# Kernel tuning notes

Hardware: AMD Instinct MI355X
Metric: run time of the kernel (lower is better)

## Reference

```python
import jax, jax.numpy as jnp
from jax import lax
import numpy as np

IMG = 1024
STRIDES = (4, 8, 16, 32, 64)
FEAT_HW = (256, 128, 64, 32, 16)
ANCHOR_SCALE = 8.0          # per-level scale multiplier of stride
RATIOS = (0.5, 1.0, 2.0)
N_ANCHOR = len(RATIOS)
PRE_NMS = 6000
POST_NMS = 300
NMS_THRESH = 0.7
MIN_SIZE = 16.0
IMG_SCALE = 1.0
NEG = -1e9


def _conv(x, w, b, pad):
    y = lax.conv_general_dilated(x, w, (1, 1), [(pad, pad), (pad, pad)],
                                 dimension_numbers=("NCHW", "OIHW", "NCHW"))
    return y + b[None, :, None, None]


def _level_anchors(H, W, stride):
    # base anchors (ymin,xmin,ymax,xmax) centered at 0, one scale per level
    r = jnp.asarray(RATIOS, jnp.float32)
    hs = stride * ANCHOR_SCALE * jnp.sqrt(r)
    ws = stride * ANCHOR_SCALE * jnp.sqrt(1.0 / r)
    base = jnp.stack([-hs / 2, -ws / 2, hs / 2, ws / 2], axis=1)  # [A,4]
    ys = jnp.arange(H, dtype=jnp.float32) * stride
    xs = jnp.arange(W, dtype=jnp.float32) * stride
    gy, gx = jnp.meshgrid(ys, xs, indexing="ij")
    shift = jnp.stack([gy, gx, gy, gx], axis=-1).reshape(-1, 1, 4)   # [HW,1,4]
    return (shift + base[None, :, :]).reshape(-1, 4)                 # [HW*A,4]


def _decode(anchors, loc):
    ah = anchors[:, 2] - anchors[:, 0]
    aw = anchors[:, 3] - anchors[:, 1]
    acy = anchors[:, 0] + 0.5 * ah
    acx = anchors[:, 1] + 0.5 * aw
    dy, dx, dh, dw = loc[:, 0], loc[:, 1], loc[:, 2], loc[:, 3]
    cy = dy * ah + acy
    cx = dx * aw + acx
    h = jnp.exp(dh) * ah
    w = jnp.exp(dw) * aw
    boxes = jnp.stack([cy - 0.5 * h, cx - 0.5 * w, cy + 0.5 * h, cx + 0.5 * w], axis=1)
    return jnp.clip(boxes, 0.0, float(IMG))


def _iou_row(box, boxes):
    ty = jnp.maximum(box[0], boxes[:, 0])
    tx = jnp.maximum(box[1], boxes[:, 1])
    by = jnp.minimum(box[2], boxes[:, 2])
    bx = jnp.minimum(box[3], boxes[:, 3])
    inter = jnp.maximum(by - ty, 0.0) * jnp.maximum(bx - tx, 0.0)
    a1 = (box[2] - box[0]) * (box[3] - box[1])
    a2 = (boxes[:, 2] - boxes[:, 0]) * (boxes[:, 3] - boxes[:, 1])
    return inter / jnp.maximum(a1 + a2 - inter, 1e-9)


def _nms(boxes, scores):
    n = boxes.shape[0]
    idx_range = jnp.arange(n)

    def body(sc, _):
        i = jnp.argmax(sc)
        valid = sc[i] > NEG / 2
        iou = _iou_row(boxes[i], boxes)
        new_sc = jnp.where((iou > NMS_THRESH) | (idx_range == i), NEG, sc)
        sc = jnp.where(valid, new_sc, sc)
        return sc, (i, valid)

    _, (idx, keep) = lax.scan(body, scores, None, length=POST_NMS)
    return boxes[idx] * keep[:, None].astype(boxes.dtype)


def reference(p2, p3, p4, p5, p6, conv_w, conv_b, loc_w, loc_b, score_w, score_b):
    feats = [p2, p3, p4, p5, p6]
    locs, fgs, anchors = [], [], []
    for f, stride in zip(feats, STRIDES):
        h = jax.nn.relu(_conv(f, conv_w, conv_b, 1))
        loc = _conv(h, loc_w, loc_b, 0)        # [1,4A,H,W]
        sc = _conv(h, score_w, score_b, 0)     # [1,2A,H,W]
        H, W = loc.shape[2], loc.shape[3]
        loc = loc.transpose(0, 2, 3, 1).reshape(-1, 4)          # [HWA,4]
        sc = sc.transpose(0, 2, 3, 1).reshape(-1, 2)            # [HWA,2]
        fgs.append(jax.nn.softmax(sc, axis=-1)[:, 1])
        locs.append(loc)
        anchors.append(_level_anchors(H, W, stride))
    loc = jnp.concatenate(locs, axis=0)
    fg = jnp.concatenate(fgs, axis=0)
    anc = jnp.concatenate(anchors, axis=0)

    boxes = _decode(anc, loc)
    hh = boxes[:, 2] - boxes[:, 0]
    ww = boxes[:, 3] - boxes[:, 1]
    min_sz = MIN_SIZE * IMG_SCALE
    fg = jnp.where((hh >= min_sz) & (ww >= min_sz), fg, NEG)

    top_scores, top_idx = lax.top_k(fg, PRE_NMS)
    top_boxes = boxes[top_idx]
    rois = _nms(top_boxes, top_scores)   # [POST_NMS,4]
    return rois


def setup_inputs() -> dict:
    key = jax.random.key(0)
    ks = jax.random.split(key, 11)
    inp = {}
    for i, (name, hw) in enumerate(zip(["p2", "p3", "p4", "p5", "p6"], FEAT_HW)):
        inp[name] = jax.random.normal(ks[i], (1, 256, hw, hw), jnp.float32)
    inp["conv_w"] = 0.01 * jax.random.normal(ks[5], (256, 256, 3, 3), jnp.float32)
    inp["conv_b"] = jnp.zeros((256,), jnp.float32)
    inp["loc_w"] = 0.01 * jax.random.normal(ks[6], (12, 256, 1, 1), jnp.float32)
    inp["loc_b"] = jnp.zeros((12,), jnp.float32)
    inp["score_w"] = 0.01 * jax.random.normal(ks[7], (6, 256, 1, 1), jnp.float32)
    inp["score_b"] = jnp.zeros((6,), jnp.float32)
    return inp
```

## Files before the change

### kernel.cpp

```cpp
#include <hip/hip_runtime.h>
#include <hip/hip_bf16.h>

typedef unsigned int u32;
typedef unsigned long long u64;
typedef float v2f __attribute__((ext_vector_type(2)));
typedef float v4f __attribute__((ext_vector_type(4)));

#define NEGV (-1000000000.0f)
#define N_ANCH 261888
#define PRE_NMS 6000
#define POST_NMS 300


__device__ __forceinline__ void gload_lds16(const float* g, float* l) {
    __builtin_amdgcn_global_load_lds((const __attribute__((address_space(1))) void*)g,
                                     (__attribute__((address_space(3))) void*)l, 16, 0, 0);
}

__device__ __forceinline__ int bucket_of(float s) {
    if (!(s > 0.0f)) return 0;
    float t = s * 4096.0f;
    int b = (int)t;
    return b > 4095 ? 4095 : b;
}

__global__ void wtrans(const float* __restrict__ cw, float* __restrict__ wt, u32* __restrict__ hist) {
    int g = blockIdx.x * 256 + threadIdx.x;
    int oc = g & 255; int cf = g >> 8;
    wt[g] = cw[oc * 2304 + cf];
    if (g < 4104) hist[g] = 0u;
}

__global__ __launch_bounds__(256, 6) void conv_head(
    const float* __restrict__ p2, const float* __restrict__ p3,
    const float* __restrict__ p4, const float* __restrict__ p5,
    const float* __restrict__ p6,
    const float* __restrict__ wt, const float* __restrict__ cb,
    const float* __restrict__ lw, const float* __restrict__ lb,
    const float* __restrict__ sw, const float* __restrict__ sb,
    float* __restrict__ scores_all, float4* __restrict__ boxes_all)
{
    __shared__ float smem[6656];
    float* Wl = smem;
    v2f*   IpL = (v2f*)(smem + 4608);
    const int tid  = threadIdx.x;
    const int wv   = tid >> 6;
    const int lane = tid & 63;

    int bid = blockIdx.x;
    const float* in; int W, stride, abase, local, lgx;
    if (bid < 2048)      { in = p2; W = 256; stride = 4;  abase = 0;      local = bid;        lgx = 6; }
    else if (bid < 2560) { in = p3; W = 128; stride = 8;  abase = 196608; local = bid - 2048; lgx = 5; }
    else if (bid < 2688) { in = p4; W = 64;  stride = 16; abase = 245760; local = bid - 2560; lgx = 4; }
    else if (bid < 2720) { in = p5; W = 32;  stride = 32; abase = 258048; local = bid - 2688; lgx = 3; }
    else                 { in = p6; W = 16;  stride = 64; abase = 261120; local = bid - 2720; lgx = 2; }
    const int bx = local & ((1 << lgx) - 1), by = local >> lgx;
    const int gx0 = bx * 4, gy0 = by * 8;
    const int HW = W * W;

    v2f acc2[4][4];
#pragma unroll
    for (int i = 0; i < 4; ++i)
#pragma unroll
        for (int j = 0; j < 4; ++j) acc2[i][j] = (v2f){0.0f, 0.0f};

    const int icw = wv & 1, halfw = wv >> 1;
    const int ee = halfw * 18 + lane;
    const int iy = ee / 6, xx = ee - iy * 6;
    const int ylo = gy0 - 1 + iy, yhi = ylo + 4, xg = gx0 - 1 + xx;
    const bool act = (lane < 18);
    const bool aLo = act && (ylo >= 0 && ylo < W && xg >= 0 && xg < W);
    const bool aHi = act && (yhi >= 0 && yhi < W && xg >= 0 && xg < W);
    const int ofsLo = ylo * W + xg;
    const int ofsHi = yhi * W + xg;
    const int ipidx = (icw * 6 + iy) * 8 + xx;

    for (int c = 0; c < 128; ++c) {
        __syncthreads();
        const float* gsrc = wt + c * 4608 + lane * 4;
#pragma unroll
        for (int k = 0; k < 5; ++k) {
            int row = wv + k * 4;
            if (row < 18) gload_lds16(gsrc + row * 256, Wl + row * 256);
        }
        const float* ibase = in + (size_t)(c * 2 + icw) * HW;
        if (act) {
            float vlo = aLo ? ibase[ofsLo] : 0.0f;
            float vhi = aHi ? ibase[ofsHi] : 0.0f;
            IpL[ipidx] = (v2f){vlo, vhi};
        }
        __syncthreads();
#pragma unroll
        for (int ic = 0; ic < 2; ++ic) {
            v2f wk2[9];
#pragma unroll
            for (int k = 0; k < 9; ++k) {
                float w_ = Wl[(ic * 9 + k) * 256 + tid];
                wk2[k] = (v2f){w_, w_};
            }
#pragma unroll
            for (int ip = 0; ip < 6; ++ip) {
                const v4f* rq = (const v4f*)&IpL[(ic * 6 + ip) * 8];
                v4f q0 = rq[0], q1 = rq[1], q2 = rq[2];
                v2f iw[6];
                iw[0] = __builtin_shufflevector(q0, q0, 0, 1);
                iw[1] = __builtin_shufflevector(q0, q0, 2, 3);
                iw[2] = __builtin_shufflevector(q1, q1, 0, 1);
                iw[3] = __builtin_shufflevector(q1, q1, 2, 3);
                iw[4] = __builtin_shufflevector(q2, q2, 0, 1);
                iw[5] = __builtin_shufflevector(q2, q2, 2, 3);
#pragma unroll
                for (int dy = 0; dy < 3; ++dy) {
                    const int tp = ip - dy;
                    if (tp >= 0 && tp < 4) {
#pragma unroll
                        for (int tx = 0; tx < 4; ++tx)
#pragma unroll
                            for (int dx = 0; dx < 3; ++dx)
                                acc2[tp][tx] = __builtin_elementwise_fma(wk2[dy * 3 + dx], iw[tx + dx], acc2[tp][tx]);
                    }
                }
            }
        }
    }
    {
        float bvv = cb[tid];
#pragma unroll
        for (int i = 0; i < 4; ++i)
#pragma unroll
            for (int j = 0; j < 4; ++j) {
                v2f t = acc2[i][j];
                t.x = fmaxf(t.x + bvv, 0.0f);
                t.y = fmaxf(t.y + bvv, 0.0f);
                acc2[i][j] = t;
            }
    }
    __syncthreads();
    float* hl = smem;
    float* ob = smem + 4160;

    for (int g = 0; g < 2; ++g) {
        __syncthreads();
#pragma unroll
        for (int p = 0; p < 16; ++p) {
            const int pr = p >> 2, tx = p & 3;
            hl[p * 260 + tid] = g ? acc2[pr][tx].y : acc2[pr][tx].x;
        }
        __syncthreads();
        for (int it = tid; it < 288; it += 256) {
            int px = it / 18, o = it - px * 18;
            float a = (o < 12) ? lb[o] : sb[o - 12];
            const float* wrow = (o < 12) ? (lw + o * 256) : (sw + (o - 12) * 256);
            const float4* hv4 = (const float4*)&hl[px * 260];
            const float4* wv4 = (const float4*)wrow;
#pragma unroll 8
            for (int cc = 0; cc < 64; ++cc) {
                float4 hv = hv4[cc], wq = wv4[cc];
                a += hv.x * wq.x; a += hv.y * wq.y; a += hv.z * wq.z; a += hv.w * wq.w;
            }
            ob[px * 20 + o] = a;
        }
        __syncthreads();
        if (tid < 48) {
            int px = tid / 3, a = tid - px * 3;
            int gy = gy0 + (g << 2) + (px >> 2);
            int gx = gx0 + (px & 3);
            float dy = ob[px * 20 + a * 4 + 0];
            float dx = ob[px * 20 + a * 4 + 1];
            float dh = ob[px * 20 + a * 4 + 2];
            float dw = ob[px * 20 + a * 4 + 3];
            float s0 = ob[px * 20 + 12 + a * 2];
            float s1 = ob[px * 20 + 13 + a * 2];
            float mm = fmaxf(s0, s1);
            float e0 = expf(s0 - mm), e1x = expf(s1 - mm);
            float fg = e1x / (e0 + e1x);
            float sqa = (a == 0) ? 0.70710678f : ((a == 1) ? 1.0f : 1.41421356f);
            float sqb = (a == 0) ? 1.41421356f : ((a == 1) ? 1.0f : 0.70710678f);
            float s8 = (float)(stride * 8);
            float hs = __fmul_rn(s8, sqa), wsz = __fmul_rn(s8, sqb);
            float g_y = (float)(gy * stride), g_x = (float)(gx * stride);
            float a_y1 = __fsub_rn(g_y, __fmul_rn(hs, 0.5f));
            float a_y2 = __fadd_rn(g_y, __fmul_rn(hs, 0.5f));
            float a_x1 = __fsub_rn(g_x, __fmul_rn(wsz, 0.5f));
            float a_x2 = __fadd_rn(g_x, __fmul_rn(wsz, 0.5f));
            float ah = __fsub_rn(a_y2, a_y1), aw = __fsub_rn(a_x2, a_x1);
            float acy = __fadd_rn(a_y1, __fmul_rn(0.5f, ah));
            float acx = __fadd_rn(a_x1, __fmul_rn(0.5f, aw));
            float cy = __fadd_rn(__fmul_rn(dy, ah), acy);
            float cx = __fadd_rn(__fmul_rn(dx, aw), acx);
            float bh = __fmul_rn(expf(dh), ah);
            float bw = __fmul_rn(expf(dw), aw);
            float y1 = __fsub_rn(cy, __fmul_rn(0.5f, bh));
            float x1 = __fsub_rn(cx, __fmul_rn(0.5f, bw));
            float y2 = __fadd_rn(cy, __fmul_rn(0.5f, bh));
            float x2 = __fadd_rn(cx, __fmul_rn(0.5f, bw));
            y1 = fminf(fmaxf(y1, 0.0f), 1024.0f); x1 = fminf(fmaxf(x1, 0.0f), 1024.0f);
            y2 = fminf(fmaxf(y2, 0.0f), 1024.0f); x2 = fminf(fmaxf(x2, 0.0f), 1024.0f);
            float hh2 = __fsub_rn(y2, y1), ww2 = __fsub_rn(x2, x1);
            float sc = (hh2 >= 16.0f && ww2 >= 16.0f) ? fg : NEGV;
            int A = abase + (gy * W + gx) * 3 + a;
            scores_all[A] = sc;
            boxes_all[A] = make_float4(y1, x1, y2, x2);
        }
    }
}

__global__ void hist_k(const float* __restrict__ scores, u32* __restrict__ hist) {
    __shared__ u32 h[4096];
    int tid = threadIdx.x;
    for (int i = tid; i < 4096; i += 256) h[i] = 0u;
    __syncthreads();
    int gid = blockIdx.x * 256 + tid;
    int gs = gridDim.x * 256;
    for (int i = gid; i < N_ANCH; i += gs)
        atomicAdd(&h[bucket_of(scores[i])], 1u);
    __syncthreads();
    for (int i = tid; i < 4096; i += 256) if (h[i]) atomicAdd(&hist[i], h[i]);
}

__global__ void select_bucket(const u32* __restrict__ hist, u32* __restrict__ cnts) {
    int lane = threadIdx.x;
    u32 S = 0;
    for (int c = 0; c < 64; ++c) {
        int bin = 4095 - (c * 64 + lane);
        u32 cnt = hist[bin];
        u32 cum = cnt;
        for (int off = 1; off < 64; off <<= 1) {
            u32 n = __shfl_up(cum, off, 64);
            if (lane >= off) cum += n;
        }
        u64 ball = __ballot(S + cum >= (u32)PRE_NMS);
        if (ball) {
            int l = __ffsll((long long)ball) - 1;
            if (lane == 0) cnts[2] = (u32)(4095 - (c * 64 + l));
            return;
        }
        S += __shfl(cum, 63, 64);
    }
    if (lane == 0) cnts[2] = 0u;
}

__global__ void compact_k(const float* __restrict__ scores, u32* __restrict__ cnts,
                          u64* __restrict__ cand) {
    int B = (int)cnts[2];
    int gid = blockIdx.x * blockDim.x + threadIdx.x;
    int gs = gridDim.x * blockDim.x;
    for (int i = gid; i < N_ANCH; i += gs) {
        float s = scores[i];
        if (bucket_of(s) >= B) {
            u32 pos = atomicAdd(&cnts[0], 1u);
            if (pos < 8192u) {
                u32 u = __float_as_uint(s);
                u32 key = (u & 0x80000000u) ? ~u : (u | 0x80000000u);
                cand[pos] = ((u64)key << 32) | (u64)((u32)(~i));
            }
        }
    }
}

__global__ __launch_bounds__(1024) void sort_gather(
    const u64* __restrict__ cand, const u32* __restrict__ cnts,
    const float* __restrict__ sall, const float4* __restrict__ ball,
    float* __restrict__ nsc, float4* __restrict__ nbx, u32* __restrict__ nvalid)
{
    __shared__ u64 srt[8192];
    int tid = threadIdx.x;
    u32 total = cnts[0]; if (total > 8192u) total = 8192u;
    for (int i = tid; i < 8192; i += 1024) srt[i] = (i < (int)total) ? cand[i] : 0ULL;
    __syncthreads();
    for (int k = 2; k <= 8192; k <<= 1) {
        for (int j = k >> 1; j > 0; j >>= 1) {
            for (int i = tid; i < 8192; i += 1024) {
                int l = i ^ j;
                if (l > i) {
                    u64 a = srt[i], b = srt[l];
                    bool descRegion = (i & k) == 0;
                    if (descRegion ? (a < b) : (a > b)) { srt[i] = b; srt[l] = a; }
                }
            }
            __syncthreads();
        }
    }
    int local = 0;
    for (int i = tid; i < PRE_NMS; i += 1024) {
        u64 comp = srt[i];
        u32 idx = ~((u32)(comp & 0xFFFFFFFFULL));
        float s; float4 bx;
        if (idx < (u32)N_ANCH) { s = sall[idx]; bx = ball[idx]; }
        else { s = NEGV; bx = make_float4(0.f, 0.f, 0.f, 0.f); }
        nsc[i] = s;
        nbx[i] = bx;
        if (s > -5.0e8f) local++;
    }
    for (int off = 32; off > 0; off >>= 1) local += __shfl_down(local, off, 64);
    if ((tid & 63) == 0) atomicAdd(nvalid, (u32)local);
}

__global__ void ioumat(const float4* __restrict__ bxs, u64* __restrict__ mat) {
    int i = blockIdx.x;
    int w = threadIdx.x;
    if (w >= 94) return;
    float4 bi = bxs[i];
    float a1 = (bi.z - bi.x) * (bi.w - bi.y);
    u64 bits = 0ULL;
    int j0 = w * 64;
    for (int b = 0; b < 64; ++b) {
        int j = j0 + b;
        if (j < PRE_NMS) {
            float4 bj = bxs[j];
            float ty = fmaxf(bi.x, bj.x), tx = fmaxf(bi.y, bj.y);
            float by = fminf(bi.z, bj.z), bx = fminf(bi.w, bj.w);
            float inter = fmaxf(by - ty, 0.0f) * fmaxf(bx - tx, 0.0f);
            float a2 = (bj.z - bj.x) * (bj.w - bj.y);
            float iou = inter / fmaxf(a1 + a2 - inter, 1e-9f);
            if (iou > 0.7f) bits |= (1ULL << b);
        }
    }
    mat[(size_t)i * 94 + w] = bits;
}

__global__ void greedy(const u64* __restrict__ mat, const float* __restrict__ nbxf,
                       const u32* __restrict__ nvalid, float* __restrict__ out) {
    int lane = threadIdx.x;
    u64 rem0 = 0ULL, rem1 = 0ULL;
    int nv = (int)*nvalid; if (nv > PRE_NMS) nv = PRE_NMS;
    int kept = 0;
    for (int widx = 0; widx * 64 < nv && kept < POST_NMS; ++widx) {
        u64 word = (widx < 64) ? __shfl(rem0, widx, 64) : __shfl(rem1, widx - 64, 64);
        int bmax = nv - widx * 64; if (bmax > 64) bmax = 64;
        for (int b = 0; b < bmax; ++b) {
            if (!((word >> b) & 1ULL)) {
                int i = widx * 64 + b;
                const u64* row = mat + (size_t)i * 94;
                rem0 |= row[lane];
                if (lane < 30) rem1 |= row[64 + lane];
                if (lane < 4) out[kept * 4 + lane] = nbxf[i * 4 + lane];
                ++kept;
                if (kept == POST_NMS) break;
                word = (widx < 64) ? __shfl(rem0, widx, 64) : __shfl(rem1, widx - 64, 64);
            }
        }
        if (kept == POST_NMS) break;
    }
    for (int idx = kept * 4 + lane; idx < POST_NMS * 4; idx += 64) out[idx] = 0.0f;
}

extern "C" void kernel_launch(void* const* d_in, const int* in_sizes, int n_in,
                              void* d_out, int out_size, void* d_ws, size_t ws_size,
                              hipStream_t stream) {
    const float* p2 = (const float*)d_in[0];
    const float* p3 = (const float*)d_in[1];
    const float* p4 = (const float*)d_in[2];
    const float* p5 = (const float*)d_in[3];
    const float* p6 = (const float*)d_in[4];
    const float* cw = (const float*)d_in[5];
    const float* cb = (const float*)d_in[6];
    const float* lw = (const float*)d_in[7];
    const float* lb = (const float*)d_in[8];
    const float* sw = (const float*)d_in[9];
    const float* sb = (const float*)d_in[10];
    float* out = (float*)d_out;
    char* ws = (char*)d_ws;

    float*  scores_all = (float*)(ws + 0);
    float4* boxes_all  = (float4*)(ws + 0x100000);
    u32*    hist       = (u32*)(ws + 0x500000);
    u32*    cnts       = (u32*)(ws + 0x504000);
    u64*    cand       = (u64*)(ws + 0x505000);
    float*  nsc        = (float*)(ws + 0x520000);
    float4* nbx        = (float4*)(ws + 0x526000);
    u64*    mat        = (u64*)(ws + 0x540000);
    float*  wt         = (float*)(ws + 0x540000);

    hipLaunchKernelGGL(wtrans, dim3(2304), dim3(256), 0, stream, cw, wt, hist);
    hipLaunchKernelGGL(conv_head, dim3(2728), dim3(256), 0, stream,
                       p2, p3, p4, p5, p6, wt, cb, lw, lb, sw, sb,
                       scores_all, boxes_all);
    hipLaunchKernelGGL(hist_k, dim3(64), dim3(256), 0, stream, scores_all, hist);
    hipLaunchKernelGGL(select_bucket, dim3(1), dim3(64), 0, stream, hist, cnts);
    hipLaunchKernelGGL(compact_k, dim3(512), dim3(256), 0, stream, scores_all, cnts, cand);
    hipLaunchKernelGGL(sort_gather, dim3(1), dim3(1024), 0, stream,
                       cand, cnts, scores_all, boxes_all, nsc, nbx, cnts + 1);
    hipLaunchKernelGGL(ioumat, dim3(PRE_NMS), dim3(128), 0, stream, nbx, mat);
    hipLaunchKernelGGL(greedy, dim3(1), dim3(64), 0, stream, mat, (const float*)nbx, cnts + 1, out);
}
```

Baseline: 1.940 ms.

## Load conv weights directly from global per thread instead of staging in LDS

```diff
diff --git a/kernel.cpp b/kernel.cpp
--- a/kernel.cpp
+++ b/kernel.cpp
@@ -11,11 +11,6 @@
 #define PRE_NMS 6000
 #define POST_NMS 300
 
-
-__device__ __forceinline__ void gload_lds16(const float* g, float* l) {
-    __builtin_amdgcn_global_load_lds((const __attribute__((address_space(1))) void*)g,
-                                     (__attribute__((address_space(3))) void*)l, 16, 0, 0);
-}
 
 __device__ __forceinline__ int bucket_of(float s) {
     if (!(s > 0.0f)) return 0;
@@ -24,10 +19,11 @@
     return b > 4095 ? 4095 : b;
 }
 
-__global__ void wtrans(const float* __restrict__ cw, float* __restrict__ wt, u32* __restrict__ hist) {
+__global__ void wtrans(const float* __restrict__ cw, float* __restrict__ wtk, u32* __restrict__ hist) {
     int g = blockIdx.x * 256 + threadIdx.x;
-    int oc = g & 255; int cf = g >> 8;
-    wt[g] = cw[oc * 2304 + cf];
+    int k = g % 12; int rest = g / 12;
+    int oc = rest & 255; int ch = rest >> 8;
+    wtk[g] = (k < 9) ? cw[oc * 2304 + ch * 9 + k] : 0.0f;
     if (g < 4104) hist[g] = 0u;
 }
 
@@ -35,14 +31,13 @@
     const float* __restrict__ p2, const float* __restrict__ p3,
     const float* __restrict__ p4, const float* __restrict__ p5,
     const float* __restrict__ p6,
-    const float* __restrict__ wt, const float* __restrict__ cb,
+    const float* __restrict__ wtk, const float* __restrict__ cb,
     const float* __restrict__ lw, const float* __restrict__ lb,
     const float* __restrict__ sw, const float* __restrict__ sb,
     float* __restrict__ scores_all, float4* __restrict__ boxes_all)
 {
     __shared__ float smem[6656];
-    float* Wl = smem;
-    v2f*   IpL = (v2f*)(smem + 4608);
+    v2f* IpL = (v2f*)(smem + 4608);
     const int tid  = threadIdx.x;
     const int wv   = tid >> 6;
     const int lane = tid & 63;
@@ -64,26 +59,18 @@
 #pragma unroll
         for (int j = 0; j < 4; ++j) acc2[i][j] = (v2f){0.0f, 0.0f};
 
-    const int icw = wv & 1, halfw = wv >> 1;
-    const int ee = halfw * 18 + lane;
-    const int iy = ee / 6, xx = ee - iy * 6;
+    const int iy = lane / 6, xx = lane - iy * 6;
     const int ylo = gy0 - 1 + iy, yhi = ylo + 4, xg = gx0 - 1 + xx;
-    const bool act = (lane < 18);
+    const bool act = (lane < 36);
     const bool aLo = act && (ylo >= 0 && ylo < W && xg >= 0 && xg < W);
     const bool aHi = act && (yhi >= 0 && yhi < W && xg >= 0 && xg < W);
     const int ofsLo = ylo * W + xg;
     const int ofsHi = yhi * W + xg;
-    const int ipidx = (icw * 6 + iy) * 8 + xx;
-
-    for (int c = 0; c < 128; ++c) {
-        __syncthreads();
-        const float* gsrc = wt + c * 4608 + lane * 4;
-#pragma unroll
-        for (int k = 0; k < 5; ++k) {
-            int row = wv + k * 4;
-            if (row < 18) gload_lds16(gsrc + row * 256, Wl + row * 256);
-        }
-        const float* ibase = in + (size_t)(c * 2 + icw) * HW;
+    const int ipidx = (wv * 6 + iy) * 8 + xx;
+
+    for (int c = 0; c < 64; ++c) {
+        __syncthreads();
+        const float* ibase = in + (size_t)(c * 4 + wv) * HW;
         if (act) {
             float vlo = aLo ? ibase[ofsLo] : 0.0f;
             float vhi = aHi ? ibase[ofsHi] : 0.0f;
@@ -91,13 +78,14 @@
         }
         __syncthreads();
 #pragma unroll
-        for (int ic = 0; ic < 2; ++ic) {
+        for (int ic = 0; ic < 4; ++ic) {
+            const int ch = c * 4 + ic;
+            const v4f* wq = (const v4f*)(wtk + (size_t)ch * 3072 + tid * 12);
+            v4f w0 = wq[0], w1 = wq[1], w2 = wq[2];
             v2f wk2[9];
-#pragma unroll
-            for (int k = 0; k < 9; ++k) {
-                float w_ = Wl[(ic * 9 + k) * 256 + tid];
-                wk2[k] = (v2f){w_, w_};
-            }
+            wk2[0] = (v2f){w0.x, w0.x}; wk2[1] = (v2f){w0.y, w0.y}; wk2[2] = (v2f){w0.z, w0.z};
+            wk2[3] = (v2f){w0.w, w0.w}; wk2[4] = (v2f){w1.x, w1.x}; wk2[5] = (v2f){w1.y, w1.y};
+            wk2[6] = (v2f){w1.z, w1.z}; wk2[7] = (v2f){w1.w, w1.w}; wk2[8] = (v2f){w2.x, w2.x};
 #pragma unroll
             for (int ip = 0; ip < 6; ++ip) {
                 const v4f* rq = (const v4f*)&IpL[(ic * 6 + ip) * 8];
@@ -135,7 +123,6 @@
                 acc2[i][j] = t;
             }
     }
-    __syncthreads();
     float* hl = smem;
     float* ob = smem + 4160;
 
@@ -370,11 +357,11 @@
     float*  nsc        = (float*)(ws + 0x520000);
     float4* nbx        = (float4*)(ws + 0x526000);
     u64*    mat        = (u64*)(ws + 0x540000);
-    float*  wt         = (float*)(ws + 0x540000);
-
-    hipLaunchKernelGGL(wtrans, dim3(2304), dim3(256), 0, stream, cw, wt, hist);
+    float*  wtk        = (float*)(ws + 0x540000);
+
+    hipLaunchKernelGGL(wtrans, dim3(3072), dim3(256), 0, stream, cw, wtk, hist);
     hipLaunchKernelGGL(conv_head, dim3(2728), dim3(256), 0, stream,
-                       p2, p3, p4, p5, p6, wt, cb, lw, lb, sw, sb,
+                       p2, p3, p4, p5, p6, wtk, cb, lw, lb, sw, sb,
                        scores_all, boxes_all);
     hipLaunchKernelGGL(hist_k, dim3(64), dim3(256), 0, stream, scores_all, hist);
     hipLaunchKernelGGL(select_bucket, dim3(1), dim3(64), 0, stream, hist, cnts);
```

Result: faster. 1.885 ms (-2.8%).
